# Performance work log

Hardware: AMD Instinct MI355X
Metric: run time of the kernel (lower is better)

Reference implementation:

```python
import jax, jax.numpy as jnp
import numpy as np

B, M, PAST, FUT, NPRED, D = 512, 32768, 8, 12, 20, 48


def _gru_step(h, x, w_ih, w_hh, b_ih, b_hh):
    # torch GRU cell: gates ordered [r, z, n]
    gi = x @ w_ih.T + b_ih
    gh = h @ w_hh.T + b_hh
    ir, iz, inn = jnp.split(gi, 3, axis=-1)
    hr, hz, hn = jnp.split(gh, 3, axis=-1)
    r = jax.nn.sigmoid(ir + hr)
    z = jax.nn.sigmoid(iz + hz)
    n = jnp.tanh(inn + r * hn)
    return (1.0 - z) * n + z * h


def setup_inputs() -> dict:
    key = jax.random.key(0)
    ks = jax.random.split(key, 16)
    f32 = jnp.float32
    def rn(k, shp, sc):
        return (jax.random.normal(k, shp, dtype=f32) * sc)
    return {
        "past": jax.random.normal(ks[0], (B, PAST, 2), dtype=f32),
        "obs_traj": jax.random.normal(ks[1], (B, PAST, 2), dtype=f32),
        "conv_w": rn(ks[2], (D, 2, 3), 0.3),
        "conv_b": jnp.zeros((D,), f32),
        "enc_w_ih": rn(ks[3], (3 * D, D), 0.1),
        "enc_w_hh": rn(ks[4], (3 * D, D), 0.1),
        "enc_b_ih": jnp.zeros((3 * D,), f32),
        "enc_b_hh": jnp.zeros((3 * D,), f32),
        "memory_past": jax.random.normal(ks[5], (M, D), dtype=f32),
        "memory_fut": jax.random.normal(ks[6], (M, D), dtype=f32),
        "Wq": rn(ks[7], (D, D), 0.1), "bq": jnp.zeros((D,), f32),
        "Wk": rn(ks[8], (D, D), 0.1), "bk": jnp.zeros((D,), f32),
        "Wv": rn(ks[9], (D, D), 0.1), "bv": jnp.zeros((D,), f32),
        "dec_w_ih": rn(ks[10], (6 * D, 2 * D), 0.1),
        "dec_w_hh": rn(ks[11], (6 * D, 2 * D), 0.1),
        "dec_b_ih": jnp.zeros((6 * D,), f32),
        "dec_b_hh": jnp.zeros((6 * D,), f32),
        "fc_w": rn(ks[12], (2, 2 * D), 0.1),
        "fc_b": jnp.zeros((2,), f32),
    }


def reference(past, obs_traj, conv_w, conv_b, enc_w_ih, enc_w_hh, enc_b_ih, enc_b_hh,
              memory_past, memory_fut, Wq, bq, Wk, bk, Wv, bv,
              dec_w_ih, dec_w_hh, dec_b_ih, dec_b_hh, fc_w, fc_b):
    b = past.shape[0]
    # --- past encoder: Conv1d(2,48,3,pad=1) + ReLU, then GRU(48,48) ---
    x = jnp.transpose(past, (0, 2, 1))                     # [B,2,T]
    emb = jax.lax.conv_general_dilated(
        x, conv_w, (1,), [(1, 1)], dimension_numbers=("NCH", "OIH", "NCH"))
    emb = jax.nn.relu(emb + conv_b[None, :, None])         # [B,48,T]
    emb = jnp.transpose(emb, (2, 0, 1))                    # [T,B,48] for scan

    def enc_step(h, x_t):
        return _gru_step(h, x_t, enc_w_ih, enc_w_hh, enc_b_ih, enc_b_hh), None
    state_past, _ = jax.lax.scan(enc_step, jnp.zeros((b, D), past.dtype), emb)  # [B,48]

    # --- iterative refinement: 20 rounds of attention over the full memory ---
    # Lin_K/Lin_V are applied to the same (full) banks every iteration -> hoist.
    K = memory_past @ Wk.T + bk                            # [M,48]
    V = memory_fut @ Wv.T + bv                             # [M,48]

    def irm_step(c, _):
        q = c @ Wq.T + bq                                  # [B,48]
        a = jax.nn.softmax(q @ K.T, axis=-1)               # [B,M], scale=1.0
        att = a @ V                                        # [B,48]
        return q + att, att
    _, atts = jax.lax.scan(irm_step, state_past, None, length=NPRED)  # [20,B,48]
    pred = jnp.transpose(atts, (1, 0, 2)).reshape(-1, D)   # [B*20,48] (b-major)

    # --- GRU(96,96) decoder, future_len steps, input only at t=0 ---
    n = b * NPRED
    present = jnp.repeat(obs_traj[:, -1], NPRED, axis=0)   # [B*20,2]
    sp = jnp.repeat(state_past, NPRED, axis=0)             # [B*20,48]
    info = jnp.concatenate([sp, pred], axis=1)             # [B*20,96]
    xs = jnp.concatenate(
        [info[None], jnp.zeros((FUT - 1, n, 2 * D), info.dtype)], axis=0)

    def dec_step(carry, x_t):
        h, pres = carry
        h = _gru_step(h, x_t, dec_w_ih, dec_w_hh, dec_b_ih, dec_b_hh)
        pres = pres + (h @ fc_w.T + fc_b)
        return (h, pres), pres
    _, coords = jax.lax.scan(
        dec_step, (jnp.zeros((n, 2 * D), info.dtype), present), xs)  # [FUT,B*20,2]

    prediction = jnp.transpose(coords, (1, 0, 2)).reshape(b, NPRED, FUT, 2)
    return prediction
```

## Files before the change

### kernel.cpp

```cpp
#include <hip/hip_runtime.h>

typedef unsigned short u16;
typedef unsigned int u32;
typedef __attribute__((ext_vector_type(8))) short short8v;
typedef __attribute__((ext_vector_type(4))) float f32x4;

#define GLD_LDS(g, l) __builtin_amdgcn_global_load_lds( \
    (const __attribute__((address_space(1))) void*)(g), \
    (__attribute__((address_space(3))) void*)(l), 16, 0, 0)

#define LOG2E 1.44269504f

__device__ __forceinline__ u16 f2bf(float f){
  union { float f; u32 u; } v; v.f = f;
  u32 r = v.u + 0x7FFFu + ((v.u >> 16) & 1u);
  return (u16)(r >> 16);
}
__device__ __forceinline__ float bf2f(u16 h){
  union { u32 u; float f; } v; v.u = ((u32)h) << 16;
  return v.f;
}
__device__ __forceinline__ u32 pk2(float a, float b){
  union { float f; u32 u; } x, y; x.f = a; y.f = b;
  return __builtin_amdgcn_perm(y.u + 0x8000u, x.u + 0x8000u, 0x07060302u);
}
__device__ __forceinline__ float sigm(float x){ return 1.f/(1.f+__expf(-x)); }
__device__ __forceinline__ float tanh_fast(float x){ return 1.f - 2.f/(1.f+__expf(2.f*x)); }

__global__ void prep_kernel(const float* dih, const float* dhh,
    const float* eih, const float* ehh, const float* wq, const float* wk, const float* wv,
    u16* Dih, u16* Dhh, u16* Eih, u16* Ehh, u16* Qf, u16* Kf, u16* Vf)
{
  int idx = blockIdx.x*256 + threadIdx.x;
  const float* src; u16* dst; int KC, Kc, e;
  if      (idx < 27648){ src=dih; dst=Dih; KC=3; Kc=96; e=idx; }
  else if (idx < 55296){ src=dhh; dst=Dhh; KC=3; Kc=96; e=idx-27648; }
  else if (idx < 64512){ src=eih; dst=Eih; KC=2; Kc=48; e=idx-55296; }
  else if (idx < 73728){ src=ehh; dst=Ehh; KC=2; Kc=48; e=idx-64512; }
  else if (idx < 76800){ src=wq;  dst=Qf;  KC=2; Kc=48; e=idx-73728; }
  else if (idx < 79872){ src=wk;  dst=Kf;  KC=2; Kc=48; e=idx-76800; }
  else if (idx < 82944){ src=wv;  dst=Vf;  KC=2; Kc=48; e=idx-79872; }
  else return;
  int j = e & 7, ln = (e>>3) & 15, qd = (e>>7) & 3, tkc = e>>9;
  int kc = tkc % KC, nt = tkc / KC;
  int g = nt*16 + ln, k = kc*32 + qd*8 + j;
  dst[e] = (k < Kc) ? f2bf(src[g*Kc + k]) : (u16)0;
}

__global__ __launch_bounds__(256) void setup_kernel(
    const float* past, const float* conv_w, const float* conv_b,
    const float* enc_b_ih, const float* enc_b_hh,
    const float* memory_past, const float* memory_fut,
    const float* bq, const float* bk, const float* bv,
    const u16* EihF, const u16* EhhF, const u16* WqF, const u16* WkF, const u16* WvF,
    float* stateP, float* qf, u16* qbB, u16* Kb, u16* Vc)
{
  __shared__ __align__(16) char SMEM[61440];
  const int tid = threadIdx.x, bx = blockIdx.x;
  const int wid = tid>>6, lane = tid&63, qd = lane>>4, ln = lane&15;
  f32x4 zf = {0.f,0.f,0.f,0.f};

  if (bx >= 504){
    int eb = bx - 504;
    u16* sWih = (u16*)(SMEM);
    u16* sWhh = (u16*)(SMEM + 18432);
    u16* sWq  = (u16*)(SMEM + 36864);
    float* sCw = (float*)(SMEM + 43008);
    float* sCb = (float*)(SMEM + 44160);
    float* sPast = (float*)(SMEM + 44352);
    u16* sHbW = (u16*)(SMEM + 48448 + wid*2304);
    for (int i = wid; i < 18; i += 4) GLD_LDS((const char*)EihF + i*1024 + lane*16, SMEM + i*1024);
    for (int i = wid; i < 18; i += 4) GLD_LDS((const char*)EhhF + i*1024 + lane*16, SMEM + 18432 + i*1024);
    for (int i = wid; i < 6;  i += 4) GLD_LDS((const char*)WqF  + i*1024 + lane*16, SMEM + 36864 + i*1024);
    for (int i = tid; i < 288; i += 256) sCw[i] = conv_w[i];
    if (tid < 48) sCb[tid] = conv_b[tid];
    for (int i = tid; i < 1024; i += 256) sPast[i] = past[eb*1024 + i];
    __syncthreads();
    short8v aE[8][2];
    {
      const float* pr = &sPast[(wid*16 + ln)*16];
      for (int t = 0; t < 8; ++t)
        for (int kc = 0; kc < 2; ++kc){
          union { short8v v; u16 h[8]; } u;
          #pragma unroll
          for (int j = 0; j < 8; ++j){
            int d = kc*32 + qd*8 + j;
            float a = 0.f;
            if (d < 48){
              a = sCb[d];
              #pragma unroll
              for (int kt = 0; kt < 3; ++kt){
                int tau = t + kt - 1;
                if (tau >= 0 && tau < 8){
                  a += pr[tau*2+0]*sCw[d*6+kt];
                  a += pr[tau*2+1]*sCw[d*6+3+kt];
                }
              }
              a = fmaxf(a, 0.f);
            }
            u.h[j] = (d < 48) ? f2bf(a) : (u16)0;
          }
          aE[t][kc] = u.v;
        }
    }
    for (int i = lane; i < 576; i += 64) ((u32*)sHbW)[i] = 0;
    float biR[3],biZ[3],biN[3],bhR[3],bhZ[3],bhN[3];
    #pragma unroll
    for (int i = 0; i < 3; ++i){
      int d = i*16 + ln;
      biR[i]=enc_b_ih[d]; biZ[i]=enc_b_ih[48+d]; biN[i]=enc_b_ih[96+d];
      bhR[i]=enc_b_hh[d]; bhZ[i]=enc_b_hh[48+d]; bhN[i]=enc_b_hh[96+d];
    }
    float hreg[3][4];
    #pragma unroll
    for (int i=0;i<3;++i) for (int r=0;r<4;++r) hreg[i][r]=0.f;
    int r0 = eb*64 + wid*16;
    #pragma unroll 1
    for (int t = 0; t < 8; ++t){
      short8v aH0 = *(const short8v*)&sHbW[ln*72 + qd*8];
      short8v aH1 = *(const short8v*)&sHbW[ln*72 + 32 + qd*8];
      f32x4 gI[9], gH[9];
      #pragma unroll
      for (int nt = 0; nt < 9; ++nt){ gI[nt] = zf; gH[nt] = zf; }
      #pragma unroll
      for (int nt = 0; nt < 9; ++nt){
        gI[nt] = __builtin_amdgcn_mfma_f32_16x16x32_bf16(aE[t][0], *(const short8v*)&sWih[((nt*2+0)*4+qd)*128 + ln*8], gI[nt], 0,0,0);
        gI[nt] = __builtin_amdgcn_mfma_f32_16x16x32_bf16(aE[t][1], *(const short8v*)&sWih[((nt*2+1)*4+qd)*128 + ln*8], gI[nt], 0,0,0);
        gH[nt] = __builtin_amdgcn_mfma_f32_16x16x32_bf16(aH0, *(const short8v*)&sWhh[((nt*2+0)*4+qd)*128 + ln*8], gH[nt], 0,0,0);
        gH[nt] = __builtin_amdgcn_mfma_f32_16x16x32_bf16(aH1, *(const short8v*)&sWhh[((nt*2+1)*4+qd)*128 + ln*8], gH[nt], 0,0,0);
      }
      #pragma unroll
      for (int i3 = 0; i3 < 3; ++i3)
        #pragma unroll
        for (int r = 0; r < 4; ++r){
          float rr = sigm(gI[i3][r]+biR[i3] + gH[i3][r]+bhR[i3]);
          float zz = sigm(gI[i3+3][r]+biZ[i3] + gH[i3+3][r]+bhZ[i3]);
          float nn = tanh_fast(gI[i3+6][r]+biN[i3] + rr*(gH[i3+6][r]+bhN[i3]));
          float hv = (1.f-zz)*nn + zz*hreg[i3][r];
          hreg[i3][r] = hv;
          sHbW[(qd*4+r)*72 + i3*16 + ln] = f2bf(hv);
        }
    }
    #pragma unroll
    for (int i3 = 0; i3 < 3; ++i3)
      #pragma unroll
      for (int r = 0; r < 4; ++r)
        stateP[(r0+qd*4+r)*48 + i3*16 + ln] = hreg[i3][r];
    short8v aH0 = *(const short8v*)&sHbW[ln*72 + qd*8];
    short8v aH1 = *(const short8v*)&sHbW[ln*72 + 32 + qd*8];
    f32x4 q3[3];
    #pragma unroll
    for (int nt = 0; nt < 3; ++nt){
      q3[nt] = zf;
      q3[nt] = __builtin_amdgcn_mfma_f32_16x16x32_bf16(aH0, *(const short8v*)&sWq[((nt*2+0)*4+qd)*128 + ln*8], q3[nt], 0,0,0);
      q3[nt] = __builtin_amdgcn_mfma_f32_16x16x32_bf16(aH1, *(const short8v*)&sWq[((nt*2+1)*4+qd)*128 + ln*8], q3[nt], 0,0,0);
    }
    #pragma unroll
    for (int nt = 0; nt < 3; ++nt)
      #pragma unroll
      for (int r = 0; r < 4; ++r){
        int row = r0 + qd*4 + r, d = nt*16 + ln;
        float v = q3[nt][r] + bq[d];
        qf[row*48 + d] = v;
        qbB[row*64 + d] = f2bf(v * LOG2E);
      }
    #pragma unroll
    for (int r = 0; r < 4; ++r)
      if (ln < 8) *(u32*)&qbB[(r0+qd*4+r)*64 + 48 + ln*2] = 0;
  } else {
    u16* sWkF = (u16*)(SMEM);
    u16* sWvF = (u16*)(SMEM + 6144);
    u16* smp  = (u16*)(SMEM + 12288 + wid*2304);
    u16* smf  = (u16*)(SMEM + 21504 + wid*2304);
    u16* sKT  = (u16*)(SMEM + 30720);
    u16* sVT  = (u16*)(SMEM + 38912);
    for (int i = wid; i < 6; i += 4) GLD_LDS((const char*)WkF + i*1024 + lane*16, SMEM + i*1024);
    for (int i = wid; i < 6; i += 4) GLD_LDS((const char*)WvF + i*1024 + lane*16, SMEM + 6144 + i*1024);
    float bkv[3], bvv[3];
    #pragma unroll
    for (int nt = 0; nt < 3; ++nt){ bkv[nt] = bk[nt*16+ln]; bvv[nt] = bv[nt*16+ln]; }
    int ntile = (bx < 8) ? 2 : 1;
    for (int tt = 0; tt < ntile; ++tt){
      int tile = (tt == 0) ? bx : (504 + bx);
      int r0 = tile*64 + wid*16;
      for (int i = lane; i < 576; i += 64){ ((u32*)smp)[i] = 0; ((u32*)smf)[i] = 0; }
      for (int i = lane; i < 768; i += 64){
        int r = i/48, c = i - r*48;
        smp[r*72+c] = f2bf(memory_past[(size_t)r0*48 + i]);
        smf[r*72+c] = f2bf(memory_fut[(size_t)r0*48 + i]);
      }
      __syncthreads();
      short8v aP0 = *(const short8v*)&smp[ln*72 + qd*8];
      short8v aP1 = *(const short8v*)&smp[ln*72 + 32 + qd*8];
      short8v aF0 = *(const short8v*)&smf[ln*72 + qd*8];
      short8v aF1 = *(const short8v*)&smf[ln*72 + 32 + qd*8];
      f32x4 k3[3], v3[3];
      #pragma unroll
      for (int nt = 0; nt < 3; ++nt){ k3[nt] = zf; v3[nt] = zf; }
      #pragma unroll
      for (int nt = 0; nt < 3; ++nt){
        k3[nt] = __builtin_amdgcn_mfma_f32_16x16x32_bf16(aP0, *(const short8v*)&sWkF[((nt*2+0)*4+qd)*128 + ln*8], k3[nt], 0,0,0);
        k3[nt] = __builtin_amdgcn_mfma_f32_16x16x32_bf16(aP1, *(const short8v*)&sWkF[((nt*2+1)*4+qd)*128 + ln*8], k3[nt], 0,0,0);
        v3[nt] = __builtin_amdgcn_mfma_f32_16x16x32_bf16(aF0, *(const short8v*)&sWvF[((nt*2+0)*4+qd)*128 + ln*8], v3[nt], 0,0,0);
        v3[nt] = __builtin_amdgcn_mfma_f32_16x16x32_bf16(aF1, *(const short8v*)&sWvF[((nt*2+1)*4+qd)*128 + ln*8], v3[nt], 0,0,0);
      }
      for (int i = lane; i < 128; i += 64) ((u32*)sKT)[(wid*16 + (i>>3))*32 + 24 + (i&7)] = 0;
      #pragma unroll
      for (int nt = 0; nt < 3; ++nt)
        #pragma unroll
        for (int r = 0; r < 4; ++r){
          int keyl = wid*16 + qd*4 + r, d = nt*16 + ln;
          sKT[keyl*64 + d] = f2bf(k3[nt][r] + bkv[nt]);
          sVT[d*72 + keyl] = f2bf(v3[nt][r] + bvv[nt]);
        }
      __syncthreads();
      for (int i = tid; i < 512; i += 256)
        *(uint4*)((char*)(Kb + (size_t)tile*64*64) + i*16) = *(const uint4*)((char*)sKT + i*16);
      for (int i = tid; i < 384; i += 256){
        int d = i>>3, sub = i&7;
        *(uint4*)((char*)(Vc + ((size_t)((tile*64)>>8)*48 + d)*256 + ((tile*64)&255)) + sub*16)
            = *(const uint4*)((char*)sVT + d*144 + sub*16);
      }
      __syncthreads();
    }
  }
}

__global__ __launch_bounds__(512) void iter_kernel(int mode, int it,
    const u16* qbB, const u16* Kb, const u16* Vc, const u16* WqF, const float* bq,
    const float* qfP, float* qfC, float* pred,
    const float* mP, const float* lP, const float* aP,
    float* mC, float* lC, float* aC)
{
  __shared__ __align__(16) char SMEM[62080];
  u16*   sQ  = (u16*)(SMEM + 51200);
  float* sWc = (float*)(SMEM + 55296);
  float* sLg = (float*)(SMEM + 57344);
  u16*   sCb = (u16*)(SMEM + 57472);
  const int tid = threadIdx.x, bx = blockIdx.x;
  const int wid = tid>>6, lane = tid&63, qd = lane>>4, ln = lane&15;
  const int rg = bx>>4, ch = bx&15;
  const int rowbase = rg*32;
  f32x4 zf = {0.f,0.f,0.f,0.f};

  if (mode == 1){
    float* sRed = (float*)SMEM;
    {
      int row = tid>>4, j = tid&15, grow = rowbase + row;
      float m = mP[grow*16 + j], l = lP[grow*16 + j];
      float mg = m;
      #pragma unroll
      for (int k = 1; k < 16; k <<= 1) mg = fmaxf(mg, __shfl_xor(mg, k));
      float w = exp2f(m - mg), wl = w*l;
      #pragma unroll
      for (int k = 1; k < 16; k <<= 1) wl += __shfl_xor(wl, k);
      sWc[row*16 + j] = w;
      if (j == 0) sLg[row] = wl;
    }
    __syncthreads();
    {
      f32x4 accv[6];
      #pragma unroll
      for (int i = 0; i < 6; ++i) accv[i] = zf;
      #pragma unroll
      for (int ci = 0; ci < 2; ++ci){
        int c = wid*2 + ci;
        const f32x4* slab = (const f32x4*)(aP + ((size_t)c*512 + rowbase)*48);
        #pragma unroll
        for (int i = 0; i < 6; ++i){
          f32x4 v = slab[i*64 + lane];
          int rr = (i*64 + lane)/12;
          float w = sWc[rr*16 + c];
          accv[i][0] += w*v[0]; accv[i][1] += w*v[1];
          accv[i][2] += w*v[2]; accv[i][3] += w*v[3];
        }
      }
      float* red = sRed + wid*1536;
      #pragma unroll
      for (int i = 0; i < 6; ++i)
        *(f32x4*)&red[(i*64 + lane)*4] = accv[i];
    }
    __syncthreads();
    for (int idx = tid; idx < 1536; idx += 512){
      float s = 0.f;
      #pragma unroll
      for (int w = 0; w < 8; ++w) s += sRed[w*1536 + idx];
      int row = idx/48, d = idx - row*48;
      float a = s / sLg[row];
      if (ch == 0) pred[(size_t)((rowbase+row)*20 + (it-1))*48 + d] = a;
      sCb[row*72 + d] = f2bf(qfP[(rowbase+row)*48 + d] + a);
    }
    if (tid < 256){ int r2 = tid>>3, p = tid&7; ((u32*)&sCb[r2*72 + 48])[p] = 0; }
    __syncthreads();
    if (wid < 2){
      short8v ac0 = *(const short8v*)&sCb[(wid*16+ln)*72 + qd*8];
      short8v ac1 = *(const short8v*)&sCb[(wid*16+ln)*72 + 32 + qd*8];
      f32x4 q3[3];
      #pragma unroll
      for (int nt = 0; nt < 3; ++nt){
        q3[nt] = zf;
        q3[nt] = __builtin_amdgcn_mfma_f32_16x16x32_bf16(ac0, *(const short8v*)&WqF[((nt*2+0)*4+qd)*128 + ln*8], q3[nt], 0,0,0);
        q3[nt] = __builtin_amdgcn_mfma_f32_16x16x32_bf16(ac1, *(const short8v*)&WqF[((nt*2+1)*4+qd)*128 + ln*8], q3[nt], 0,0,0);
      }
      #pragma unroll
      for (int nt = 0; nt < 3; ++nt)
        #pragma unroll
        for (int r = 0; r < 4; ++r){
          int lr = wid*16 + qd*4 + r, d = nt*16 + ln;
          float v = q3[nt][r] + bq[d];
          if (ch == 0) qfC[(rowbase + lr)*48 + d] = v;
          sQ[lr*64 + d] = f2bf(v * LOG2E);
        }
    } else if (wid < 4){
      for (int i = tid-128; i < 256; i += 128){
        int r2 = i>>3, p = i&7;
        ((u32*)&sQ[r2*64 + 48])[p] = 0;
      }
    }
    __syncthreads();
  } else {
    const u32* src = (const u32*)(qbB + rowbase*64);
    ((u32*)sQ)[tid] = src[tid];
    ((u32*)sQ)[512 + tid] = src[512 + tid];
    __syncthreads();
  }

  u16* sp8 = (u16*)SMEM + wid*2304;
  short8v aq[2][2];
  #pragma unroll
  for (int rt = 0; rt < 2; ++rt)
    #pragma unroll
    for (int kc = 0; kc < 2; ++kc)
      aq[rt][kc] = *(const short8v*)&sQ[(rt*16+ln)*64 + kc*32 + qd*8];
  f32x4 acc[2][3];
  #pragma unroll
  for (int rt = 0; rt < 2; ++rt) for (int dt = 0; dt < 3; ++dt) acc[rt][dt] = zf;
  float mrun[2] = {-3.0e38f, -3.0e38f}, lrun[2] = {0.f, 0.f};
  u16* spb[2] = { sp8, sp8 + 1152 };
  const int wslice = ch*2048 + wid*256;

  #pragma unroll
  for (int kt = 0; kt < 4; ++kt){
    const int tb = wslice + kt*64;
    const u16* kb = Kb + (size_t)tb*64;
    const u16* vb = Vc + (size_t)(tb>>8)*48*256 + (tb & 255);
    short8v kf[4][2], vf[2][3];
    #pragma unroll
    for (int nt = 0; nt < 4; ++nt)
      #pragma unroll
      for (int kc = 0; kc < 2; ++kc)
        kf[nt][kc] = *(const short8v*)&kb[(nt*16+ln)*64 + kc*32 + qd*8];
    #pragma unroll
    for (int kc = 0; kc < 2; ++kc)
      #pragma unroll
      for (int dt = 0; dt < 3; ++dt)
        vf[kc][dt] = *(const short8v*)&vb[(dt*16+ln)*256 + kc*32 + qd*8];
    f32x4 s[2][4];
    #pragma unroll
    for (int rt = 0; rt < 2; ++rt)
      #pragma unroll
      for (int nt = 0; nt < 4; ++nt){
        f32x4 z = zf;
        z = __builtin_amdgcn_mfma_f32_16x16x32_bf16(kf[nt][0], aq[rt][0], z, 0,0,0);
        z = __builtin_amdgcn_mfma_f32_16x16x32_bf16(kf[nt][1], aq[rt][1], z, 0,0,0);
        s[rt][nt] = z;
      }
    #pragma unroll
    for (int rt = 0; rt < 2; ++rt){
      float vmax = fmaxf(fmaxf(fmaxf(s[rt][0][0], s[rt][0][1]), fmaxf(s[rt][0][2], s[rt][0][3])),
                   fmaxf(fmaxf(s[rt][1][0], s[rt][1][1]), fmaxf(s[rt][1][2], s[rt][1][3])));
      vmax = fmaxf(vmax, fmaxf(fmaxf(fmaxf(s[rt][2][0], s[rt][2][1]), fmaxf(s[rt][2][2], s[rt][2][3])),
                   fmaxf(fmaxf(s[rt][3][0], s[rt][3][1]), fmaxf(s[rt][3][2], s[rt][3][3]))));
      vmax = fmaxf(vmax, __shfl_xor(vmax, 16));
      vmax = fmaxf(vmax, __shfl_xor(vmax, 32));
      float mnew = fmaxf(mrun[rt], vmax);
      float alpha = exp2f(mrun[rt] - mnew);
      mrun[rt] = mnew;
      u16* sp = spb[rt];
      float lsum = 0.f;
      #pragma unroll
      for (int nt = 0; nt < 4; ++nt){
        float p0 = exp2f(s[rt][nt][0]-mnew), p1 = exp2f(s[rt][nt][1]-mnew);
        float p2 = exp2f(s[rt][nt][2]-mnew), p3 = exp2f(s[rt][nt][3]-mnew);
        lsum += (p0+p1)+(p2+p3);
        uint2 pk; pk.x = pk2(p0,p1); pk.y = pk2(p2,p3);
        *(uint2*)&sp[ln*72 + nt*16 + qd*4] = pk;
      }
      lsum += __shfl_xor(lsum, 16);
      lsum += __shfl_xor(lsum, 32);
      lrun[rt] = lrun[rt]*alpha + lsum;
      #pragma unroll
      for (int dt = 0; dt < 3; ++dt){
        acc[rt][dt][0] *= alpha; acc[rt][dt][1] *= alpha;
        acc[rt][dt][2] *= alpha; acc[rt][dt][3] *= alpha;
      }
      short8v pb0 = *(const short8v*)&sp[ln*72 + qd*8];
      short8v pb1 = *(const short8v*)&sp[ln*72 + 32 + qd*8];
      #pragma unroll
      for (int dt = 0; dt < 3; ++dt){
        acc[rt][dt] = __builtin_amdgcn_mfma_f32_16x16x32_bf16(vf[0][dt], pb0, acc[rt][dt], 0,0,0);
        acc[rt][dt] = __builtin_amdgcn_mfma_f32_16x16x32_bf16(vf[1][dt], pb1, acc[rt][dt], 0,0,0);
      }
    }
  }
  __syncthreads();
  float* sMg = (float*)SMEM;
  #pragma unroll
  for (int rt = 0; rt < 2; ++rt)
    #pragma unroll
    for (int dt = 0; dt < 3; ++dt)
      #pragma unroll
      for (int r = 0; r < 4; ++r)
        sMg[wid*1600 + (rt*16+ln)*50 + dt*16 + qd*4 + r] = acc[rt][dt][r];
  if (lane < 16){
    sMg[wid*1600 + ln*50 + 48] = mrun[0]; sMg[wid*1600 + ln*50 + 49] = lrun[0];
    sMg[wid*1600 + (16+ln)*50 + 48] = mrun[1]; sMg[wid*1600 + (16+ln)*50 + 49] = lrun[1];
  }
  __syncthreads();
  {
    int row = tid>>4, jj = tid&15, grow = rowbase + row;
    float mg = -3.0e38f, mv[8];
    #pragma unroll
    for (int w = 0; w < 8; ++w){ mv[w] = sMg[w*1600 + row*50 + 48]; mg = fmaxf(mg, mv[w]); }
    float ev[8], lg = 0.f;
    #pragma unroll
    for (int w = 0; w < 8; ++w){ ev[w] = exp2f(mv[w]-mg); lg += ev[w]*sMg[w*1600 + row*50 + 49]; }
    if (jj == 0){ mC[grow*16 + ch] = mg; lC[grow*16 + ch] = lg; }
    int d0 = jj*3;
    #pragma unroll
    for (int d3 = 0; d3 < 3; ++d3){
      int d = d0 + d3;
      float s = 0.f;
      #pragma unroll
      for (int w = 0; w < 8; ++w) s += ev[w]*sMg[w*1600 + row*50 + d];
      aC[((size_t)ch*512 + grow)*48 + d] = s;
    }
  }
}

__global__ __launch_bounds__(384) void dec_kernel(
    const u16* Dihf, const u16* Dhhf, const float* b_ih, const float* b_hh,
    const float* stateP, const float* pred, const float* obs,
    const float* mF, const float* lF, const float* aF,
    const float* fc_w, const float* fc_b, float* out)
{
  __shared__ __align__(16) u16 sx[2][16*104];
  __shared__ float sPx[2][6][16], sPy[2][6][16];
  const int tid = threadIdx.x, bx = blockIdx.x;
  const int wid = tid>>6, lane = tid&63, qd = lane>>4, ln = lane&15;
  const int rw = bx*16;
  f32x4 zf = {0.f,0.f,0.f,0.f};

  for (int i = tid; i < 1536; i += 384){
    int r = i/96, k = i - r*96;
    int row = rw + r, b20 = row/20;
    float v = (k < 48) ? stateP[b20*48 + k] : pred[(size_t)row*48 + (k-48)];
    sx[0][r*104 + k] = f2bf(v);
  }
  if (tid < 48){
    int r19 = (19 - (rw % 20)) % 20;
    if (r19 < 16){
      int b = (rw + r19)/20;
      float mg = -3.0e38f, mv[16];
      #pragma unroll
      for (int c = 0; c < 16; ++c){ mv[c] = mF[b*16 + c]; mg = fmaxf(mg, mv[c]); }
      float num = 0.f, den = 0.f;
      #pragma unroll
      for (int c = 0; c < 16; ++c){
        float w = exp2f(mv[c] - mg);
        den += w * lF[b*16 + c];
        num += w * aF[((size_t)c*512 + b)*48 + tid];
      }
      sx[0][r19*104 + 48 + tid] = f2bf(num/den);
    }
  }
  short8v whh[3][3];
  #pragma unroll
  for (int g = 0; g < 3; ++g)
    #pragma unroll
    for (int kc = 0; kc < 3; ++kc)
      whh[g][kc] = *(const short8v*)&Dhhf[(((g*6+wid)*3+kc)*4+qd)*128 + ln*8];
  const int d = wid*16 + ln;
  float biR=b_ih[d], biZ=b_ih[96+d], biN=b_ih[192+d];
  float bhR=b_hh[d], bhZ=b_hh[96+d], bhN=b_hh[192+d];
  float fw0=fc_w[d], fw1=fc_w[96+d];
  float hold[4] = {0.f,0.f,0.f,0.f};
  float fcb0 = fc_b[0], fcb1 = fc_b[1];
  float pres0 = 0.f, pres1 = 0.f;
  if (wid == 0 && lane < 16){
    int b20 = (rw + lane)/20;
    pres0 = obs[b20*16 + 14];
    pres1 = obs[b20*16 + 15];
  }
  __syncthreads();

  #pragma unroll 1
  for (int t = 0; t < 12; ++t){
    const u16* sr = sx[t&1];
    u16* sw = sx[(t+1)&1];
    short8v xa0 = *(const short8v*)&sr[ln*104 + qd*8];
    short8v xa1 = *(const short8v*)&sr[ln*104 + 32 + qd*8];
    short8v xa2 = *(const short8v*)&sr[ln*104 + 64 + qd*8];
    f32x4 acc[3] = {zf, zf, zf};
    if (t == 0){
      #pragma unroll
      for (int g = 0; g < 3; ++g){
        int nt = g*6 + wid;
        acc[g] = __builtin_amdgcn_mfma_f32_16x16x32_bf16(xa0, *(const short8v*)&Dihf[((nt*3+0)*4+qd)*128 + ln*8], acc[g], 0,0,0);
        acc[g] = __builtin_amdgcn_mfma_f32_16x16x32_bf16(xa1, *(const short8v*)&Dihf[((nt*3+1)*4+qd)*128 + ln*8], acc[g], 0,0,0);
        acc[g] = __builtin_amdgcn_mfma_f32_16x16x32_bf16(xa2, *(const short8v*)&Dihf[((nt*3+2)*4+qd)*128 + ln*8], acc[g], 0,0,0);
      }
    } else {
      #pragma unroll
      for (int g = 0; g < 3; ++g){
        acc[g] = __builtin_amdgcn_mfma_f32_16x16x32_bf16(xa0, whh[g][0], acc[g], 0,0,0);
        acc[g] = __builtin_amdgcn_mfma_f32_16x16x32_bf16(xa1, whh[g][1], acc[g], 0,0,0);
        acc[g] = __builtin_amdgcn_mfma_f32_16x16x32_bf16(xa2, whh[g][2], acc[g], 0,0,0);
      }
    }
    float px[4], py[4];
    #pragma unroll
    for (int r = 0; r < 4; ++r){
      float rr = sigm(acc[0][r] + biR + bhR);
      float zz = sigm(acc[1][r] + biZ + bhZ);
      float nn = (t == 0) ? tanh_fast(acc[2][r] + biN + rr*bhN)
                          : tanh_fast(biN + rr*(acc[2][r] + bhN));
      float hv = (1.f-zz)*nn + zz*hold[r];
      hold[r] = hv;
      sw[(qd*4+r)*104 + d] = f2bf(hv);
      px[r] = fw0*hv;
      py[r] = fw1*hv;
    }
    #pragma unroll
    for (int msk = 8; msk >= 1; msk >>= 1)
      #pragma unroll
      for (int r = 0; r < 4; ++r){
        px[r] += __shfl_xor(px[r], msk);
        py[r] += __shfl_xor(py[r], msk);
      }
    if (ln == 0){
      #pragma unroll
      for (int r = 0; r < 4; ++r){
        sPx[t&1][wid][qd*4+r] = px[r];
        sPy[t&1][wid][qd*4+r] = py[r];
      }
    }
    __syncthreads();
    if (wid == 0 && lane < 16){
      float fx = 0.f, fy = 0.f;
      #pragma unroll
      for (int w = 0; w < 6; ++w){ fx += sPx[t&1][w][lane]; fy += sPy[t&1][w][lane]; }
      pres0 += fx + fcb0;
      pres1 += fy + fcb1;
      out[((size_t)(rw + lane)*12 + t)*2 + 0] = pres0;
      out[((size_t)(rw + lane)*12 + t)*2 + 1] = pres1;
    }
  }
}

extern "C" void kernel_launch(void* const* d_in, const int* in_sizes, int n_in,
                              void* d_out, int out_size, void* d_ws, size_t ws_size,
                              hipStream_t stream)
{
  const float* past        = (const float*)d_in[0];
  const float* obs         = (const float*)d_in[1];
  const float* conv_w      = (const float*)d_in[2];
  const float* conv_b      = (const float*)d_in[3];
  const float* enc_w_ih    = (const float*)d_in[4];
  const float* enc_w_hh    = (const float*)d_in[5];
  const float* enc_b_ih    = (const float*)d_in[6];
  const float* enc_b_hh    = (const float*)d_in[7];
  const float* memory_past = (const float*)d_in[8];
  const float* memory_fut  = (const float*)d_in[9];
  const float* Wq = (const float*)d_in[10];
  const float* bq = (const float*)d_in[11];
  const float* Wk = (const float*)d_in[12];
  const float* bk = (const float*)d_in[13];
  const float* Wv = (const float*)d_in[14];
  const float* bv = (const float*)d_in[15];
  const float* dec_w_ih = (const float*)d_in[16];
  const float* dec_w_hh = (const float*)d_in[17];
  const float* dec_b_ih = (const float*)d_in[18];
  const float* dec_b_hh = (const float*)d_in[19];
  const float* fc_w = (const float*)d_in[20];
  const float* fc_b = (const float*)d_in[21];
  float* out = (float*)d_out;

  char* ws = (char*)d_ws;
  size_t off = 0;
  auto alloc = [&](size_t bytes){ void* p = ws + off; off += (bytes + 255) & ~(size_t)255; return p; };
  float* stateP = (float*)alloc(512*48*4);
  float* qfA    = (float*)alloc(512*48*4);
  float* qfB    = (float*)alloc(512*48*4);
  u16*   qbB    = (u16*)alloc(512*64*2);
  float* mB[2], *lB[2], *aB[2];
  for (int i = 0; i < 2; ++i){
    mB[i] = (float*)alloc(512*16*4);
    lB[i] = (float*)alloc(512*16*4);
    aB[i] = (float*)alloc((size_t)512*16*48*4);
  }
  float* pred = (float*)alloc((size_t)10240*48*4);
  u16*   Kb   = (u16*)alloc((size_t)32768*64*2);
  u16*   Vc   = (u16*)alloc((size_t)32768*48*2);
  u16*   Dihf = (u16*)alloc(27648*2);
  u16*   Dhhf = (u16*)alloc(27648*2);
  u16*   EihF = (u16*)alloc(9216*2);
  u16*   EhhF = (u16*)alloc(9216*2);
  u16*   WqF  = (u16*)alloc(3072*2);
  u16*   WkF  = (u16*)alloc(3072*2);
  u16*   WvF  = (u16*)alloc(3072*2);
  float* qbuf[2] = { qfA, qfB };

  prep_kernel<<<324, 256, 0, stream>>>(dec_w_ih, dec_w_hh, enc_w_ih, enc_w_hh,
                                       Wq, Wk, Wv, Dihf, Dhhf, EihF, EhhF, WqF, WkF, WvF);

  setup_kernel<<<512, 256, 0, stream>>>(
      past, conv_w, conv_b, enc_b_ih, enc_b_hh, memory_past, memory_fut,
      bq, bk, bv, EihF, EhhF, WqF, WkF, WvF,
      stateP, qfA, qbB, Kb, Vc);

  iter_kernel<<<256, 512, 0, stream>>>(0, 0, qbB, Kb, Vc, WqF, bq,
      qfA, qfA, pred, mB[1], lB[1], aB[1], mB[0], lB[0], aB[0]);
  for (int it = 1; it < 20; ++it){
    int pv = (it-1)&1, cu = it&1;
    iter_kernel<<<256, 512, 0, stream>>>(1, it, qbB, Kb, Vc, WqF, bq,
        qbuf[pv], qbuf[cu], pred, mB[pv], lB[pv], aB[pv], mB[cu], lB[cu], aB[cu]);
  }

  dec_kernel<<<640, 384, 0, stream>>>(Dihf, Dhhf, dec_b_ih, dec_b_hh,
      stateP, pred, obs, mB[1], lB[1], aB[1], fc_w, fc_b, out);
}
```

Baseline: 626.3 us.

## Halve iter_kernel waves per block, doubling key tiles per wave

```diff
diff --git a/kernel.cpp b/kernel.cpp
--- a/kernel.cpp
+++ b/kernel.cpp
@@ -226,17 +226,17 @@
   }
 }
 
-__global__ __launch_bounds__(512) void iter_kernel(int mode, int it,
+__global__ __launch_bounds__(256, 1) void iter_kernel(int mode, int it,
     const u16* qbB, const u16* Kb, const u16* Vc, const u16* WqF, const float* bq,
     const float* qfP, float* qfC, float* pred,
     const float* mP, const float* lP, const float* aP,
     float* mC, float* lC, float* aC)
 {
-  __shared__ __align__(16) char SMEM[62080];
-  u16*   sQ  = (u16*)(SMEM + 51200);
-  float* sWc = (float*)(SMEM + 55296);
-  float* sLg = (float*)(SMEM + 57344);
-  u16*   sCb = (u16*)(SMEM + 57472);
+  __shared__ __align__(16) char SMEM[55936];
+  u16*   sQ  = (u16*)(SMEM + 45056);
+  float* sWc = (float*)(SMEM + 49152);
+  float* sLg = (float*)(SMEM + 51200);
+  u16*   sCb = (u16*)(SMEM + 51332);
   const int tid = threadIdx.x, bx = blockIdx.x;
   const int wid = tid>>6, lane = tid&63, qd = lane>>4, ln = lane&15;
   const int rg = bx>>4, ch = bx&15;
@@ -246,16 +246,18 @@
   if (mode == 1){
     float* sRed = (float*)SMEM;
     {
-      int row = tid>>4, j = tid&15, grow = rowbase + row;
-      float m = mP[grow*16 + j], l = lP[grow*16 + j];
-      float mg = m;
-      #pragma unroll
-      for (int k = 1; k < 16; k <<= 1) mg = fmaxf(mg, __shfl_xor(mg, k));
-      float w = exp2f(m - mg), wl = w*l;
-      #pragma unroll
-      for (int k = 1; k < 16; k <<= 1) wl += __shfl_xor(wl, k);
-      sWc[row*16 + j] = w;
-      if (j == 0) sLg[row] = wl;
+      int row = tid>>3, jj = tid&7, grow = rowbase + row;
+      float m0 = mP[grow*16 + jj*2], m1 = mP[grow*16 + jj*2+1];
+      float l0 = lP[grow*16 + jj*2], l1 = lP[grow*16 + jj*2+1];
+      float mg = fmaxf(m0, m1);
+      #pragma unroll
+      for (int k = 1; k < 8; k <<= 1) mg = fmaxf(mg, __shfl_xor(mg, k));
+      float w0 = exp2f(m0 - mg), w1 = exp2f(m1 - mg);
+      float wl = w0*l0 + w1*l1;
+      #pragma unroll
+      for (int k = 1; k < 8; k <<= 1) wl += __shfl_xor(wl, k);
+      sWc[row*16 + jj*2] = w0; sWc[row*16 + jj*2+1] = w1;
+      if (jj == 0) sLg[row] = wl;
     }
     __syncthreads();
     {
@@ -263,8 +265,8 @@
       #pragma unroll
       for (int i = 0; i < 6; ++i) accv[i] = zf;
       #pragma unroll
-      for (int ci = 0; ci < 2; ++ci){
-        int c = wid*2 + ci;
+      for (int ci = 0; ci < 4; ++ci){
+        int c = wid*4 + ci;
         const f32x4* slab = (const f32x4*)(aP + ((size_t)c*512 + rowbase)*48);
         #pragma unroll
         for (int i = 0; i < 6; ++i){
@@ -281,16 +283,20 @@
         *(f32x4*)&red[(i*64 + lane)*4] = accv[i];
     }
     __syncthreads();
-    for (int idx = tid; idx < 1536; idx += 512){
-      float s = 0.f;
-      #pragma unroll
-      for (int w = 0; w < 8; ++w) s += sRed[w*1536 + idx];
-      int row = idx/48, d = idx - row*48;
-      float a = s / sLg[row];
-      if (ch == 0) pred[(size_t)((rowbase+row)*20 + (it-1))*48 + d] = a;
-      sCb[row*72 + d] = f2bf(qfP[(rowbase+row)*48 + d] + a);
-    }
-    if (tid < 256){ int r2 = tid>>3, p = tid&7; ((u32*)&sCb[r2*72 + 48])[p] = 0; }
+    {
+      int row = tid>>3, jj = tid&7, grow = rowbase + row;
+      float lg = sLg[row];
+      int base = row*48 + jj*6;
+      #pragma unroll
+      for (int d6 = 0; d6 < 6; ++d6){
+        int d = jj*6 + d6;
+        float s = sRed[base+d6] + sRed[1536+base+d6] + sRed[3072+base+d6] + sRed[4608+base+d6];
+        float a = s / lg;
+        if (ch == 0) pred[(size_t)(grow*20 + (it-1))*48 + d] = a;
+        sCb[row*72 + d] = f2bf(qfP[grow*48 + d] + a);
+      }
+      ((u32*)&sCb[row*72 + 48])[jj] = 0;
+    }
     __syncthreads();
     if (wid < 2){
       short8v ac0 = *(const short8v*)&sCb[(wid*16+ln)*72 + qd*8];
@@ -311,7 +317,7 @@
           if (ch == 0) qfC[(rowbase + lr)*48 + d] = v;
           sQ[lr*64 + d] = f2bf(v * LOG2E);
         }
-    } else if (wid < 4){
+    } else {
       for (int i = tid-128; i < 256; i += 128){
         int r2 = i>>3, p = i&7;
         ((u32*)&sQ[r2*64 + 48])[p] = 0;
@@ -320,12 +326,15 @@
     __syncthreads();
   } else {
     const u32* src = (const u32*)(qbB + rowbase*64);
-    ((u32*)sQ)[tid] = src[tid];
+    ((u32*)sQ)[tid]       = src[tid];
+    ((u32*)sQ)[256 + tid] = src[256 + tid];
     ((u32*)sQ)[512 + tid] = src[512 + tid];
+    ((u32*)sQ)[768 + tid] = src[768 + tid];
     __syncthreads();
   }
 
-  u16* sp8 = (u16*)SMEM + wid*2304;
+  const int wslice = ch*2048 + wid*512;
+  u16* sp8 = (u16*)(SMEM + 26624);
   short8v aq[2][2];
   #pragma unroll
   for (int rt = 0; rt < 2; ++rt)
@@ -336,11 +345,10 @@
   #pragma unroll
   for (int rt = 0; rt < 2; ++rt) for (int dt = 0; dt < 3; ++dt) acc[rt][dt] = zf;
   float mrun[2] = {-3.0e38f, -3.0e38f}, lrun[2] = {0.f, 0.f};
-  u16* spb[2] = { sp8, sp8 + 1152 };
-  const int wslice = ch*2048 + wid*256;
+  u16* spb[2] = { sp8 + (wid*2+0)*1152, sp8 + (wid*2+1)*1152 };
 
   #pragma unroll
-  for (int kt = 0; kt < 4; ++kt){
+  for (int kt = 0; kt < 8; ++kt){
     const int tb = wslice + kt*64;
     const u16* kb = Kb + (size_t)tb*64;
     const u16* vb = Vc + (size_t)(tb>>8)*48*256 + (tb & 255);
@@ -418,33 +426,32 @@
   }
   __syncthreads();
   {
-    int row = tid>>4, jj = tid&15, grow = rowbase + row;
-    float mg = -3.0e38f, mv[8];
-    #pragma unroll
-    for (int w = 0; w < 8; ++w){ mv[w] = sMg[w*1600 + row*50 + 48]; mg = fmaxf(mg, mv[w]); }
-    float ev[8], lg = 0.f;
-    #pragma unroll
-    for (int w = 0; w < 8; ++w){ ev[w] = exp2f(mv[w]-mg); lg += ev[w]*sMg[w*1600 + row*50 + 49]; }
+    int row = tid>>3, jj = tid&7, grow = rowbase + row;
+    float m0 = sMg[row*50+48], m1 = sMg[1600+row*50+48];
+    float m2 = sMg[3200+row*50+48], m3 = sMg[4800+row*50+48];
+    float mg = fmaxf(fmaxf(m0,m1), fmaxf(m2,m3));
+    float e0 = exp2f(m0-mg), e1 = exp2f(m1-mg), e2 = exp2f(m2-mg), e3 = exp2f(m3-mg);
+    float lg = e0*sMg[row*50+49] + e1*sMg[1600+row*50+49]
+             + e2*sMg[3200+row*50+49] + e3*sMg[4800+row*50+49];
     if (jj == 0){ mC[grow*16 + ch] = mg; lC[grow*16 + ch] = lg; }
-    int d0 = jj*3;
-    #pragma unroll
-    for (int d3 = 0; d3 < 3; ++d3){
-      int d = d0 + d3;
-      float s = 0.f;
-      #pragma unroll
-      for (int w = 0; w < 8; ++w) s += ev[w]*sMg[w*1600 + row*50 + d];
-      aC[((size_t)ch*512 + grow)*48 + d] = s;
-    }
-  }
-}
-
-__global__ __launch_bounds__(384) void dec_kernel(
+    int d0 = jj*6;
+    #pragma unroll
+    for (int d6 = 0; d6 < 6; ++d6){
+      int d = d0 + d6;
+      aC[((size_t)ch*512 + grow)*48 + d] =
+          e0*sMg[row*50+d] + e1*sMg[1600+row*50+d]
+        + e2*sMg[3200+row*50+d] + e3*sMg[4800+row*50+d];
+    }
+  }
+}
+
+__global__ __launch_bounds__(384, 1) void dec_kernel(
     const u16* Dihf, const u16* Dhhf, const float* b_ih, const float* b_hh,
     const float* stateP, const float* pred, const float* obs,
     const float* mF, const float* lF, const float* aF,
     const float* fc_w, const float* fc_b, float* out)
 {
-  __shared__ __align__(16) u16 sx[2][16*104];
+  __shared__ __align__(16) u16 sx[2][16*106];
   __shared__ float sPx[2][6][16], sPy[2][6][16];
   const int tid = threadIdx.x, bx = blockIdx.x;
   const int wid = tid>>6, lane = tid&63, qd = lane>>4, ln = lane&15;
@@ -455,7 +462,7 @@
     int r = i/96, k = i - r*96;
     int row = rw + r, b20 = row/20;
     float v = (k < 48) ? stateP[b20*48 + k] : pred[(size_t)row*48 + (k-48)];
-    sx[0][r*104 + k] = f2bf(v);
+    sx[0][r*106 + k] = f2bf(v);
   }
   if (tid < 48){
     int r19 = (19 - (rw % 20)) % 20;
@@ -471,7 +478,7 @@
         den += w * lF[b*16 + c];
         num += w * aF[((size_t)c*512 + b)*48 + tid];
       }
-      sx[0][r19*104 + 48 + tid] = f2bf(num/den);
+      sx[0][r19*106 + 48 + tid] = f2bf(num/den);
     }
   }
   short8v whh[3][3];
@@ -498,9 +505,9 @@
   for (int t = 0; t < 12; ++t){
     const u16* sr = sx[t&1];
     u16* sw = sx[(t+1)&1];
-    short8v xa0 = *(const short8v*)&sr[ln*104 + qd*8];
-    short8v xa1 = *(const short8v*)&sr[ln*104 + 32 + qd*8];
-    short8v xa2 = *(const short8v*)&sr[ln*104 + 64 + qd*8];
+    short8v xa0 = *(const short8v*)&sr[ln*106 + qd*8];
+    short8v xa1 = *(const short8v*)&sr[ln*106 + 32 + qd*8];
+    short8v xa2 = *(const short8v*)&sr[ln*106 + 64 + qd*8];
     f32x4 acc[3] = {zf, zf, zf};
     if (t == 0){
       #pragma unroll
@@ -527,7 +534,7 @@
                           : tanh_fast(biN + rr*(acc[2][r] + bhN));
       float hv = (1.f-zz)*nn + zz*hold[r];
       hold[r] = hv;
-      sw[(qd*4+r)*104 + d] = f2bf(hv);
+      sw[(qd*4+r)*106 + d] = f2bf(hv);
       px[r] = fw0*hv;
       py[r] = fw1*hv;
     }
@@ -619,11 +626,11 @@
       bq, bk, bv, EihF, EhhF, WqF, WkF, WvF,
       stateP, qfA, qbB, Kb, Vc);
 
-  iter_kernel<<<256, 512, 0, stream>>>(0, 0, qbB, Kb, Vc, WqF, bq,
+  iter_kernel<<<256, 256, 0, stream>>>(0, 0, qbB, Kb, Vc, WqF, bq,
       qfA, qfA, pred, mB[1], lB[1], aB[1], mB[0], lB[0], aB[0]);
   for (int it = 1; it < 20; ++it){
     int pv = (it-1)&1, cu = it&1;
-    iter_kernel<<<256, 512, 0, stream>>>(1, it, qbB, Kb, Vc, WqF, bq,
+    iter_kernel<<<256, 256, 0, stream>>>(1, it, qbB, Kb, Vc, WqF, bq,
         qbuf[pv], qbuf[cu], pred, mB[pv], lB[pv], aB[pv], mB[cu], lB[cu], aB[cu]);
   }
 
```

Result: no change. 628.7 us (+0.4%).
